# Kernel tuning notes

Hardware: AMD Instinct MI355X
Metric: run time of the kernel (lower is better)

## Reference

```python
import jax, jax.numpy as jnp
import numpy as np

B = 4096      # batch rows
T = 8192      # hop_length (time steps per call)
N = 256       # n_taps = len(b)


def setup_inputs() -> dict:
    key = jax.random.key(0)
    kx, kb, kz = jax.random.split(key, 3)
    x = jax.random.normal(kx, (B, T), dtype=jnp.float32)
    # FIR coefficients (nn.Parameter b in the torch module)
    b = jax.random.normal(kb, (N,), dtype=jnp.float32) / N
    # 'zeros_init' is an nn.Parameter initialized to zeros but learned; use small
    # nonzero values so its contribution to the math is exercised.
    zeros_init = jax.random.normal(kz, (N, T), dtype=jnp.float32) * 0.01
    return {"x": x, "b": b, "zeros_init": zeros_init}


def reference(x, b, zeros_init):
    # Torch module semantics: per-step the recurrence keeps a length-N buffer
    #   buff_t = [x_t, buff_{t-1}[0:N-1]]            (shift-in, drop oldest)
    #   y_t    = sum_k b[k] * buff_t[k] = sum_k b[k] * x_{t-k}
    # with initial buffer buff_{-1} = x @ zeros_init.T, i.e. zi[:, j] plays the
    # role of x_{-1-j} for j = 0..N-2 (zi[:, N-1] is shifted out before use).
    # This is exactly a causal FIR / depthwise 1-D convolution, which we fuse
    # into a single valid convolution over an extended signal.
    n = b.shape[0]
    zi = x @ zeros_init.T                       # [B, N] initial buffer
    hist = jnp.flip(zi[:, : n - 1], axis=-1)    # [B, N-1]: x_{-(N-1)} .. x_{-1}
    x_ext = jnp.concatenate([hist, x], axis=-1)  # [B, T + N - 1]
    # lax conv is cross-correlation: out[t] = sum_j k[j] * in[t+j];
    # we need out[t] = sum_k b[k] * x_ext[t + N-1 - k]  ->  kernel = flip(b).
    y = jax.lax.conv_general_dilated(
        x_ext[:, None, :],                      # [B, 1, T+N-1]  (NCW)
        jnp.flip(b)[None, None, :],             # [1, 1, N]      (OIW)
        window_strides=(1,),
        padding="VALID",
    )
    return y[:, 0, :]                           # [B, T]
```

## Files before the change

kernel.cpp:

```cpp
#include <hip/hip_runtime.h>
#include <hip/hip_bf16.h>

#define B_ROWS 4096
#define T_LEN  8192
#define N_TAPS 256

typedef __attribute__((ext_vector_type(8))) short short8;
typedef __attribute__((ext_vector_type(4))) short short4v;
typedef __attribute__((ext_vector_type(4))) float f32x4;

__device__ inline ushort f2bf(float f) {
    __hip_bfloat16 h = __float2bfloat16(f);
    union { __hip_bfloat16 h; ushort u; } c;
    c.h = h;
    return c.u;
}

__global__ __launch_bounds__(256) void fir_cast_z(const float* __restrict__ z,
                                                  ushort* __restrict__ zbf) {
    const int idx = (blockIdx.x * 256 + threadIdx.x) * 8;
    float4 a = *(const float4*)&z[idx];
    float4 b = *(const float4*)&z[idx + 4];
    short8 o;
    o[0] = (short)f2bf(a.x); o[1] = (short)f2bf(a.y);
    o[2] = (short)f2bf(a.z); o[3] = (short)f2bf(a.w);
    o[4] = (short)f2bf(b.x); o[5] = (short)f2bf(b.y);
    o[6] = (short)f2bf(b.z); o[7] = (short)f2bf(b.w);
    *(short8*)&zbf[idx] = o;
}

__global__ void fir_build_wtab(const float* __restrict__ b,
                               ushort* __restrict__ wtab) {
    const int a = blockIdx.x;
    const int lane = threadIdx.x;
    const int l15 = lane & 15, lg = lane >> 4;
    short8 o;
    #pragma unroll
    for (int j = 0; j < 8; ++j) {
        const int bi = 16 * a - 32 + l15 - lg * 8 - j;
        const float v = (bi >= 0 && bi < N_TAPS) ? b[bi] : 0.f;
        o[j] = (short)f2bf(v);
    }
    *(short8*)&wtab[(a * 64 + lane) * 8] = o;
}

#define MT 128
#define GBK 64

__global__ __launch_bounds__(512) void fir_zi_gemm(const float* __restrict__ x,
                                                   const ushort* __restrict__ zbf,
                                                   float* __restrict__ part,
                                                   int kslices) {
    __shared__ ushort As[MT * GBK];
    __shared__ ushort Bs[N_TAPS * GBK];
    const int i0 = blockIdx.x * MT;
    const int ks = blockIdx.y;
    const int klen = T_LEN / kslices;
    const int kbase = ks * klen;
    const int tid = threadIdx.x;
    const int wid = tid >> 6, lane = tid & 63;
    const int wm = wid >> 2, wn = wid & 3;
    const int l15 = lane & 15, lg = lane >> 4;

    f32x4 acc[4][4];
    #pragma unroll
    for (int mi = 0; mi < 4; ++mi)
        #pragma unroll
        for (int ni = 0; ni < 4; ++ni) acc[mi][ni] = (f32x4){0.f, 0.f, 0.f, 0.f};

    for (int kc = 0; kc < klen; kc += GBK) {
        #pragma unroll
        for (int q = 0; q < 4; ++q) {
            const int e = tid + q * 512;
            const int r = e >> 4;
            const int c4 = (e & 15) * 4;
            float4 v = *(const float4*)&x[(size_t)(i0 + r) * T_LEN + kbase + kc + c4];
            short4v o;
            o[0] = (short)f2bf(v.x); o[1] = (short)f2bf(v.y);
            o[2] = (short)f2bf(v.z); o[3] = (short)f2bf(v.w);
            const int boff = r * 128 + ((c4 * 2) ^ ((r & 7) << 4));
            *(short4v*)((char*)As + boff) = o;
        }
        #pragma unroll
        for (int q = 0; q < 4; ++q) {
            const int e = tid + q * 512;
            const int r = e >> 3;
            const int c8 = (e & 7) * 8;
            short8 v = *(const short8*)&zbf[(size_t)r * T_LEN + kbase + kc + c8];
            const int boff = r * 128 + ((c8 * 2) ^ ((r & 7) << 4));
            *(short8*)((char*)Bs + boff) = v;
        }
        __syncthreads();
        #pragma unroll
        for (int ksb = 0; ksb < 2; ++ksb) {
            short8 af[4], bfr[4];
            const int cb = (lg * 8 + ksb * 32) * 2;
            #pragma unroll
            for (int mi = 0; mi < 4; ++mi) {
                const int row = wm * 64 + mi * 16 + l15;
                af[mi] = *(const short8*)((const char*)As + row * 128 + (cb ^ ((row & 7) << 4)));
            }
            #pragma unroll
            for (int ni = 0; ni < 4; ++ni) {
                const int row = wn * 64 + ni * 16 + l15;
                bfr[ni] = *(const short8*)((const char*)Bs + row * 128 + (cb ^ ((row & 7) << 4)));
            }
            #pragma unroll
            for (int mi = 0; mi < 4; ++mi)
                #pragma unroll
                for (int ni = 0; ni < 4; ++ni)
                    acc[mi][ni] = __builtin_amdgcn_mfma_f32_16x16x32_bf16(
                        af[mi], bfr[ni], acc[mi][ni], 0, 0, 0);
        }
        __syncthreads();
    }

    #pragma unroll
    for (int mi = 0; mi < 4; ++mi) {
        #pragma unroll
        for (int ni = 0; ni < 4; ++ni) {
            const int gn = wn * 64 + ni * 16 + l15;
            #pragma unroll
            for (int rg = 0; rg < 4; ++rg) {
                const int gm = i0 + wm * 64 + mi * 16 + lg * 4 + rg;
                part[((size_t)ks * B_ROWS + gm) * N_TAPS + gn] = acc[mi][ni][rg];
            }
        }
    }
}

__global__ __launch_bounds__(256) void fir_zi_reduce(const float* __restrict__ part,
                                                     float* __restrict__ zi,
                                                     int kslices) {
    const int idx = blockIdx.x * 256 + threadIdx.x;
    const int total = B_ROWS * N_TAPS / 4;
    if (idx >= total) return;
    float4 s = ((const float4*)part)[idx];
    for (int q = 1; q < kslices; ++q) {
        float4 v = ((const float4*)part)[(size_t)q * total + idx];
        s.x += v.x; s.y += v.y; s.z += v.z; s.w += v.w;
    }
    ((float4*)zi)[idx] = s;
}

#define VBM 16
#define VBT 1024
#define VWIN 1280
#define VSTR 2560

__global__ __launch_bounds__(256, 2) void fir_conv_mfma(
        const float* __restrict__ x,
        const ushort* __restrict__ wtab,
        const float* __restrict__ zi,
        float* __restrict__ y) {
    __shared__ ushort xe[VBM * VSTR / 2];
    const int t0 = blockIdx.x * VBT;
    const int i0 = blockIdx.y * VBM;
    const int tid = threadIdx.x;
    const int lane = tid & 63, wid = tid >> 6;
    const int l15 = lane & 15, lg = lane >> 4;

    short8 wf[18];
    #pragma unroll
    for (int a = 0; a < 18; ++a)
        wf[a] = *(const short8*)&wtab[((a + 2) * 64 + lane) * 8];

    #pragma unroll
    for (int it = 0; it < 8; ++it) {
        const int e = tid + it * 256;
        const int r = e >> 7;
        const int c8 = e & 127;
        const int g = t0 + c8 * 8;
        float4 v0 = *(const float4*)&x[(size_t)(i0 + r) * T_LEN + g];
        float4 v1 = *(const float4*)&x[(size_t)(i0 + r) * T_LEN + g + 4];
        short8 o;
        o[0] = (short)f2bf(v0.x); o[1] = (short)f2bf(v0.y);
        o[2] = (short)f2bf(v0.z); o[3] = (short)f2bf(v0.w);
        o[4] = (short)f2bf(v1.x); o[5] = (short)f2bf(v1.y);
        o[6] = (short)f2bf(v1.z); o[7] = (short)f2bf(v1.w);
        const int off = (512 + c8 * 16) ^ ((r & 7) << 4);
        *(short8*)((char*)xe + r * VSTR + off) = o;
    }
    #pragma unroll
    for (int it = 0; it < 2; ++it) {
        const int e = tid + it * 256;
        const int r = e >> 5;
        const int c8 = e & 31;
        const int g = t0 - 256 + c8 * 8;
        short8 o;
        if (g >= 0) {
            float4 v0 = *(const float4*)&x[(size_t)(i0 + r) * T_LEN + g];
            float4 v1 = *(const float4*)&x[(size_t)(i0 + r) * T_LEN + g + 4];
            o[0] = (short)f2bf(v0.x); o[1] = (short)f2bf(v0.y);
            o[2] = (short)f2bf(v0.z); o[3] = (short)f2bf(v0.w);
            o[4] = (short)f2bf(v1.x); o[5] = (short)f2bf(v1.y);
            o[6] = (short)f2bf(v1.z); o[7] = (short)f2bf(v1.w);
        } else {
            #pragma unroll
            for (int jj = 0; jj < 8; ++jj)
                o[jj] = (short)f2bf(zi[(size_t)(i0 + r) * N_TAPS + (-1 - g - jj)]);
        }
        const int off = (c8 * 16) ^ ((r & 7) << 4);
        *(short8*)((char*)xe + r * VSTR + off) = o;
    }
    __syncthreads();

    f32x4 acc[4][4];
    #pragma unroll
    for (int c4 = 0; c4 < 4; ++c4)
        #pragma unroll
        for (int n = 0; n < 4; ++n) acc[c4][n] = (f32x4){0.f, 0.f, 0.f, 0.f};

    const int chunk0 = wid * 4;
    #pragma unroll
    for (int ui = 0; ui < 10; ++ui) {
        #pragma unroll
        for (int c4 = 0; c4 < 4; ++c4) {
            const int colw = (chunk0 + c4) * 64 + ui * 32 + lg * 8;
            const int off = (colw * 2) ^ ((l15 & 7) << 4);
            short8 af = *(const short8*)((const char*)xe + l15 * VSTR + off);
            #pragma unroll
            for (int ncol = 0; ncol < 4; ++ncol) {
                const int a = ncol + 18 - 2 * ui;
                if (a >= 2 && a <= 19)
                    acc[c4][ncol] = __builtin_amdgcn_mfma_f32_16x16x32_bf16(
                        af, wf[a - 2], acc[c4][ncol], 0, 0, 0);
            }
        }
    }

    #pragma unroll
    for (int c4 = 0; c4 < 4; ++c4) {
        #pragma unroll
        for (int ncol = 0; ncol < 4; ++ncol) {
            const size_t tcol = (size_t)t0 + (chunk0 + c4) * 64 + ncol * 16 + l15;
            #pragma unroll
            for (int rg = 0; rg < 4; ++rg) {
                y[(size_t)(i0 + lg * 4 + rg) * T_LEN + tcol] = acc[c4][ncol][rg];
            }
        }
    }
}

extern "C" void kernel_launch(void* const* d_in, const int* in_sizes, int n_in,
                              void* d_out, int out_size, void* d_ws, size_t ws_size,
                              hipStream_t stream) {
    const float* x  = (const float*)d_in[0];
    const float* b  = (const float*)d_in[1];
    const float* z  = (const float*)d_in[2];
    float* y = (float*)d_out;

    char* ws = (char*)d_ws;
    float*  zi   = (float*)ws;
    ushort* zbf  = (ushort*)(ws + (4u << 20));
    ushort* wtab = (ushort*)(ws + (8u << 20));
    float*  part = (float*)(ws + (8u << 20) + (64u << 10));

    int kslices = 8;
    while (kslices > 1 &&
           (size_t)(8u << 20) + (64u << 10) + (size_t)kslices * (4u << 20) > ws_size)
        kslices >>= 1;

    fir_build_wtab<<<22, 64, 0, stream>>>(b, wtab);
    fir_cast_z<<<N_TAPS * T_LEN / (256 * 8), 256, 0, stream>>>(z, zbf);

    dim3 ggrid(B_ROWS / MT, kslices);
    fir_zi_gemm<<<ggrid, 512, 0, stream>>>(x, zbf, part, kslices);

    fir_zi_reduce<<<B_ROWS * N_TAPS / 4 / 256, 256, 0, stream>>>(part, zi, kslices);

    dim3 cgrid(T_LEN / VBT, B_ROWS / VBM);
    fir_conv_mfma<<<cgrid, 256, 0, stream>>>(x, wtab, zi, y);
}
```

Baseline: 127.0 us.

## Double-buffer zi GEMM tiles with async global-to-LDS loads for B

Adds ping-pong shared-memory buffers to the zi GEMM. The next K tile is prefetched while the current one is computed: A goes through registers with the bf16 conversion and store delayed until after the MFMAs, and B is copied straight into LDS via global_load_lds. This removes one barrier per iteration and hides global load latency behind the matrix math. The cost is twice the LDS footprint, which may cut occupancy, plus extra registers held by the A prefetch.

Result: faster. 110.3 us (-13.2%).

```diff
diff --git a/kernel.cpp b/kernel.cpp
--- a/kernel.cpp
+++ b/kernel.cpp
@@ -14,6 +14,12 @@
     union { __hip_bfloat16 h; ushort u; } c;
     c.h = h;
     return c.u;
+}
+
+typedef __attribute__((address_space(1))) const void g_void;
+typedef __attribute__((address_space(3))) void s_void;
+__device__ inline void gload16(const void* g, void* s) {
+    __builtin_amdgcn_global_load_lds((g_void*)g, (s_void*)s, 16, 0, 0);
 }
 
 __global__ __launch_bounds__(256) void fir_cast_z(const float* __restrict__ z,
@@ -46,13 +52,15 @@
 
 #define MT 128
 #define GBK 64
+#define ASZ (MT * GBK)
+#define BSZ (N_TAPS * GBK)
 
 __global__ __launch_bounds__(512) void fir_zi_gemm(const float* __restrict__ x,
                                                    const ushort* __restrict__ zbf,
                                                    float* __restrict__ part,
                                                    int kslices) {
-    __shared__ ushort As[MT * GBK];
-    __shared__ ushort Bs[N_TAPS * GBK];
+    __shared__ ushort As[2 * ASZ];
+    __shared__ ushort Bs[2 * BSZ];
     const int i0 = blockIdx.x * MT;
     const int ks = blockIdx.y;
     const int klen = T_LEN / kslices;
@@ -62,35 +70,64 @@
     const int wm = wid >> 2, wn = wid & 3;
     const int l15 = lane & 15, lg = lane >> 4;
 
+    const int a_r0 = tid >> 4;
+    const int a_c4 = (tid & 15) * 4;
+    const int b_rl = lane >> 3;
+    const int b_c  = lane & 7;
+
     f32x4 acc[4][4];
     #pragma unroll
     for (int mi = 0; mi < 4; ++mi)
         #pragma unroll
         for (int ni = 0; ni < 4; ++ni) acc[mi][ni] = (f32x4){0.f, 0.f, 0.f, 0.f};
 
-    for (int kc = 0; kc < klen; kc += GBK) {
+    const int nt = klen / GBK;
+
+    float4 apf[4];
+
+    auto issueA = [&](int kc) {
         #pragma unroll
         for (int q = 0; q < 4; ++q) {
-            const int e = tid + q * 512;
-            const int r = e >> 4;
-            const int c4 = (e & 15) * 4;
-            float4 v = *(const float4*)&x[(size_t)(i0 + r) * T_LEN + kbase + kc + c4];
+            const int r = a_r0 + q * 32;
+            apf[q] = *(const float4*)&x[(size_t)(i0 + r) * T_LEN + kbase + kc + a_c4];
+        }
+    };
+    auto issueB = [&](int kc, int buf) {
+        #pragma unroll
+        for (int q = 0; q < 4; ++q) {
+            const int row = q * 64 + wid * 8 + b_rl;
+            const int gc  = b_c ^ (row & 7);
+            const void* g = &zbf[(size_t)row * T_LEN + kbase + kc + gc * 8];
+            void* s = (char*)&Bs[buf * BSZ] + (q * 8 + wid) * 1024;
+            gload16(g, s);
+        }
+    };
+    auto writeA = [&](int buf) {
+        #pragma unroll
+        for (int q = 0; q < 4; ++q) {
+            const int r = a_r0 + q * 32;
             short4v o;
-            o[0] = (short)f2bf(v.x); o[1] = (short)f2bf(v.y);
-            o[2] = (short)f2bf(v.z); o[3] = (short)f2bf(v.w);
-            const int boff = r * 128 + ((c4 * 2) ^ ((r & 7) << 4));
-            *(short4v*)((char*)As + boff) = o;
-        }
-        #pragma unroll
-        for (int q = 0; q < 4; ++q) {
-            const int e = tid + q * 512;
-            const int r = e >> 3;
-            const int c8 = (e & 7) * 8;
-            short8 v = *(const short8*)&zbf[(size_t)r * T_LEN + kbase + kc + c8];
-            const int boff = r * 128 + ((c8 * 2) ^ ((r & 7) << 4));
-            *(short8*)((char*)Bs + boff) = v;
-        }
-        __syncthreads();
+            o[0] = (short)f2bf(apf[q].x); o[1] = (short)f2bf(apf[q].y);
+            o[2] = (short)f2bf(apf[q].z); o[3] = (short)f2bf(apf[q].w);
+            const int boff = r * 128 + ((a_c4 * 2) ^ ((r & 7) << 4));
+            *(short4v*)((char*)&As[buf * ASZ] + boff) = o;
+        }
+    };
+
+    issueA(0);
+    issueB(0, 0);
+    writeA(0);
+    __syncthreads();
+
+    int cur = 0;
+    for (int t = 0; t < nt; ++t) {
+        const int pf = (t + 1 < nt);
+        if (pf) {
+            issueA((t + 1) * GBK);
+            issueB((t + 1) * GBK, cur ^ 1);
+        }
+        const char* Ab = (const char*)&As[cur * ASZ];
+        const char* Bb = (const char*)&Bs[cur * BSZ];
         #pragma unroll
         for (int ksb = 0; ksb < 2; ++ksb) {
             short8 af[4], bfr[4];
@@ -98,12 +135,12 @@
             #pragma unroll
             for (int mi = 0; mi < 4; ++mi) {
                 const int row = wm * 64 + mi * 16 + l15;
-                af[mi] = *(const short8*)((const char*)As + row * 128 + (cb ^ ((row & 7) << 4)));
+                af[mi] = *(const short8*)(Ab + row * 128 + (cb ^ ((row & 7) << 4)));
             }
             #pragma unroll
             for (int ni = 0; ni < 4; ++ni) {
                 const int row = wn * 64 + ni * 16 + l15;
-                bfr[ni] = *(const short8*)((const char*)Bs + row * 128 + (cb ^ ((row & 7) << 4)));
+                bfr[ni] = *(const short8*)(Bb + row * 128 + (cb ^ ((row & 7) << 4)));
             }
             #pragma unroll
             for (int mi = 0; mi < 4; ++mi)
@@ -112,7 +149,9 @@
                     acc[mi][ni] = __builtin_amdgcn_mfma_f32_16x16x32_bf16(
                         af[mi], bfr[ni], acc[mi][ni], 0, 0, 0);
         }
+        if (pf) writeA(cur ^ 1);
         __syncthreads();
+        cur ^= 1;
     }
 
     #pragma unroll
```

## Register-prefetch next K tile in zi GEMM and shrink block to 64 rows

Applied to the files above, without the earlier changes.

The zi GEMM now uses 64-row tiles with 256 threads (4 waves each covering all 64 rows and a 64-column slice) and launch bounds allowing two blocks per CU. Global loads for the next K tile are issued into registers before the MFMA work on the current tile, then stored to LDS at the start of the next iteration. This is meant to hide global-load latency and raise occupancy. The cost is more registers for the prefetch buffers, twice as many blocks, and the z tile being reloaded by twice as many blocks.

Result: faster. 105.6 us (-16.8%).

```diff
diff --git a/kernel.cpp b/kernel.cpp
--- a/kernel.cpp
+++ b/kernel.cpp
@@ -44,13 +44,14 @@
     *(short8*)&wtab[(a * 64 + lane) * 8] = o;
 }
 
-#define MT 128
+#define MT 64
 #define GBK 64
 
-__global__ __launch_bounds__(512) void fir_zi_gemm(const float* __restrict__ x,
-                                                   const ushort* __restrict__ zbf,
-                                                   float* __restrict__ part,
-                                                   int kslices) {
+__global__ __launch_bounds__(256, 2) void fir_zi_gemm(
+        const float* __restrict__ x,
+        const ushort* __restrict__ zbf,
+        float* __restrict__ part,
+        int kslices) {
     __shared__ ushort As[MT * GBK];
     __shared__ ushort Bs[N_TAPS * GBK];
     const int i0 = blockIdx.x * MT;
@@ -58,38 +59,63 @@
     const int klen = T_LEN / kslices;
     const int kbase = ks * klen;
     const int tid = threadIdx.x;
-    const int wid = tid >> 6, lane = tid & 63;
-    const int wm = wid >> 2, wn = wid & 3;
+    const int wn = tid >> 6;
+    const int lane = tid & 63;
     const int l15 = lane & 15, lg = lane >> 4;
 
+    const int a_r = tid >> 4;
+    const int a_c4 = (tid & 15) * 4;
+    const int b_r0 = tid >> 3;
+    const int b_c8 = (tid & 7) * 8;
+
     f32x4 acc[4][4];
     #pragma unroll
     for (int mi = 0; mi < 4; ++mi)
         #pragma unroll
         for (int ni = 0; ni < 4; ++ni) acc[mi][ni] = (f32x4){0.f, 0.f, 0.f, 0.f};
 
-    for (int kc = 0; kc < klen; kc += GBK) {
+    const int nt = klen / GBK;
+
+    float4 apf[4];
+    short8 bpf[8];
+
+    auto loadT = [&](int kc) {
         #pragma unroll
         for (int q = 0; q < 4; ++q) {
-            const int e = tid + q * 512;
-            const int r = e >> 4;
-            const int c4 = (e & 15) * 4;
-            float4 v = *(const float4*)&x[(size_t)(i0 + r) * T_LEN + kbase + kc + c4];
+            const int r = a_r;
+            apf[q] = *(const float4*)&x[(size_t)(i0 + a_r + q * 16) * T_LEN
+                                        + kbase + kc + a_c4];
+            (void)r;
+        }
+        #pragma unroll
+        for (int q = 0; q < 8; ++q) {
+            bpf[q] = *(const short8*)&zbf[(size_t)(b_r0 + q * 32) * T_LEN
+                                          + kbase + kc + b_c8];
+        }
+    };
+    auto storeT = [&]() {
+        #pragma unroll
+        for (int q = 0; q < 4; ++q) {
+            const int r = a_r + q * 16;
             short4v o;
-            o[0] = (short)f2bf(v.x); o[1] = (short)f2bf(v.y);
-            o[2] = (short)f2bf(v.z); o[3] = (short)f2bf(v.w);
-            const int boff = r * 128 + ((c4 * 2) ^ ((r & 7) << 4));
+            o[0] = (short)f2bf(apf[q].x); o[1] = (short)f2bf(apf[q].y);
+            o[2] = (short)f2bf(apf[q].z); o[3] = (short)f2bf(apf[q].w);
+            const int boff = r * 128 + ((a_c4 * 2) ^ ((r & 7) << 4));
             *(short4v*)((char*)As + boff) = o;
         }
         #pragma unroll
-        for (int q = 0; q < 4; ++q) {
-            const int e = tid + q * 512;
-            const int r = e >> 3;
-            const int c8 = (e & 7) * 8;
-            short8 v = *(const short8*)&zbf[(size_t)r * T_LEN + kbase + kc + c8];
-            const int boff = r * 128 + ((c8 * 2) ^ ((r & 7) << 4));
-            *(short8*)((char*)Bs + boff) = v;
-        }
+        for (int q = 0; q < 8; ++q) {
+            const int r = b_r0 + q * 32;
+            const int boff = r * 128 + ((b_c8 * 2) ^ ((r & 7) << 4));
+            *(short8*)((char*)Bs + boff) = bpf[q];
+        }
+    };
+
+    loadT(0);
+    for (int t = 0; t < nt; ++t) {
+        __syncthreads();
+        storeT();
+        if (t + 1 < nt) loadT((t + 1) * GBK);
         __syncthreads();
         #pragma unroll
         for (int ksb = 0; ksb < 2; ++ksb) {
@@ -97,13 +123,15 @@
             const int cb = (lg * 8 + ksb * 32) * 2;
             #pragma unroll
             for (int mi = 0; mi < 4; ++mi) {
-                const int row = wm * 64 + mi * 16 + l15;
-                af[mi] = *(const short8*)((const char*)As + row * 128 + (cb ^ ((row & 7) << 4)));
+                const int row = mi * 16 + l15;
+                af[mi] = *(const short8*)((const char*)As + row * 128
+                                          + (cb ^ ((row & 7) << 4)));
             }
             #pragma unroll
             for (int ni = 0; ni < 4; ++ni) {
                 const int row = wn * 64 + ni * 16 + l15;
-                bfr[ni] = *(const short8*)((const char*)Bs + row * 128 + (cb ^ ((row & 7) << 4)));
+                bfr[ni] = *(const short8*)((const char*)Bs + row * 128
+                                           + (cb ^ ((row & 7) << 4)));
             }
             #pragma unroll
             for (int mi = 0; mi < 4; ++mi)
@@ -112,7 +140,6 @@
                     acc[mi][ni] = __builtin_amdgcn_mfma_f32_16x16x32_bf16(
                         af[mi], bfr[ni], acc[mi][ni], 0, 0, 0);
         }
-        __syncthreads();
     }
 
     #pragma unroll
@@ -122,7 +149,7 @@
             const int gn = wn * 64 + ni * 16 + l15;
             #pragma unroll
             for (int rg = 0; rg < 4; ++rg) {
-                const int gm = i0 + wm * 64 + mi * 16 + lg * 4 + rg;
+                const int gm = i0 + mi * 16 + lg * 4 + rg;
                 part[((size_t)ks * B_ROWS + gm) * N_TAPS + gn] = acc[mi][ni][rg];
             }
         }
@@ -265,7 +292,7 @@
     fir_cast_z<<<N_TAPS * T_LEN / (256 * 8), 256, 0, stream>>>(z, zbf);
 
     dim3 ggrid(B_ROWS / MT, kslices);
-    fir_zi_gemm<<<ggrid, 512, 0, stream>>>(x, zbf, part, kslices);
+    fir_zi_gemm<<<ggrid, 256, 0, stream>>>(x, zbf, part, kslices);
 
     fir_zi_reduce<<<B_ROWS * N_TAPS / 4 / 256, 256, 0, stream>>>(part, zi, kslices);
 
```
